# Optimization experiments

Measured on AMD Instinct MI355X. Metric: run time of the kernel, lower is better.

Reference implementation:

```python
import jax, jax.numpy as jnp
import numpy as np

NUM_HEADS = 16
NEG = -1e9

def setup_inputs() -> dict:
    key = jax.random.key(0)
    ks = jax.random.split(key, 5)
    B, S, D = 4, 2048, 1024
    scale = 1.0 / np.sqrt(D)
    return {
        "x": jax.random.normal(ks[0], (B, S, D), dtype=jnp.float32),
        "WQ": jax.random.normal(ks[1], (D, D), dtype=jnp.float32) * scale,
        "WK": jax.random.normal(ks[2], (D, D), dtype=jnp.float32) * scale,
        "WV": jax.random.normal(ks[3], (D, D), dtype=jnp.float32) * scale,
        "WO": jax.random.normal(ks[4], (D, D), dtype=jnp.float32) * scale,
    }

def _split_heads(t, h):
    # [..., s, h*d] -> [..., h, s, d]
    *lead, s, hd = t.shape
    return jnp.swapaxes(t.reshape(*lead, s, h, hd // h), -3, -2)

def reference(x, WQ, WK, WV, WO):
    h = NUM_HEADS
    S = x.shape[-2]
    # Linear stores weight [out, in]; y = x @ W^T
    Q = _split_heads(x @ WQ.T, h)  # [b,h,s,dk]
    K = _split_heads(x @ WK.T, h)
    V = _split_heads(x @ WV.T, h)
    dk = Q.shape[-1]
    scores = jnp.einsum('bhqd,bhkd->bhqk', Q, K) / jnp.sqrt(jnp.float32(dk))
    causal = jnp.tril(jnp.ones((S, S), dtype=bool))  # allowed positions
    scores = jnp.where(causal, scores, NEG)
    # explicit stable softmax (matches source)
    m = jnp.max(scores, axis=-1, keepdims=True)
    e = jnp.exp(scores - m)
    attn = e / jnp.sum(e, axis=-1, keepdims=True)
    out = jnp.einsum('bhqk,bhkd->bhqd', attn, V)  # [b,h,s,dv]
    out = jnp.swapaxes(out, -3, -2).reshape(*x.shape[:-1], -1)  # [b,s,h*dv]
    return out @ WO.T
```

## Files before the change

### kernel.cpp

```cpp
#include <hip/hip_runtime.h>
#include <stdint.h>
#include <math.h>

typedef __attribute__((ext_vector_type(8))) short bf16x8;
typedef __attribute__((ext_vector_type(4))) short v4s;
typedef __attribute__((ext_vector_type(4))) float f32x4;
typedef __attribute__((ext_vector_type(4))) unsigned short u16x4;
typedef __attribute__((ext_vector_type(2))) unsigned int u32x2;

#define MFMA16(a,b,c)   __builtin_amdgcn_mfma_f32_16x16x32_bf16((a),(b),(c),0,0,0)
#define MFMA16K(a,b,c)  __builtin_amdgcn_mfma_f32_16x16x16bf16_1k((a),(b),(c),0,0,0)

static __device__ __forceinline__ void gld_lds16(const void* g, void* l) {
  __builtin_amdgcn_global_load_lds(
      (const __attribute__((address_space(1))) unsigned int*)g,
      (__attribute__((address_space(3))) unsigned int*)l,
      16, 0, 0);
}

static __device__ __forceinline__ unsigned short f2bf(float f) {
  unsigned int u = __builtin_bit_cast(unsigned int, f);
  return (unsigned short)((u + 0x8000u) >> 16);
}

__global__ __launch_bounds__(256) void cvt_kernel(const float* __restrict__ in,
                                                  unsigned short* __restrict__ out,
                                                  int n4) {
  int i = blockIdx.x * blockDim.x + threadIdx.x;
  int stride = gridDim.x * blockDim.x;
  for (; i < n4; i += stride) {
    float4 v = ((const float4*)in)[i];
    u16x4 o;
    o.x = f2bf(v.x); o.y = f2bf(v.y); o.z = f2bf(v.z); o.w = f2bf(v.w);
    ((u16x4*)out)[i] = o;
  }
}

__global__ __launch_bounds__(256) void cvt4_kernel(const float* __restrict__ w0,
                                                   const float* __restrict__ w1,
                                                   const float* __restrict__ w2,
                                                   const float* __restrict__ w3,
                                                   unsigned short* __restrict__ out) {
  const float* in = (blockIdx.y == 0) ? w0 : (blockIdx.y == 1) ? w1
                  : (blockIdx.y == 2) ? w2 : w3;
  unsigned short* o = out + (size_t)blockIdx.y * 1048576;
  int i = blockIdx.x * blockDim.x + threadIdx.x;
  int stride = gridDim.x * blockDim.x;
  for (; i < 1048576/4; i += stride) {
    float4 v = ((const float4*)in)[i];
    u16x4 t;
    t.x = f2bf(v.x); t.y = f2bf(v.y); t.z = f2bf(v.z); t.w = f2bf(v.w);
    ((u16x4*)o)[i] = t;
  }
}

template<int MODE, typename CT>
__device__ __forceinline__ void gemm_bt_tile(const unsigned short* __restrict__ A,
                                             const unsigned short* __restrict__ Bt,
                                             CT* __restrict__ C,
                                             int m0, int n0)
{
  __shared__ __align__(16) unsigned short As[128*32];
  __shared__ __align__(16) unsigned short Bs[128*32];
  const int tid  = threadIdx.x;
  const int w    = tid >> 6, lane = tid & 63;
  const int quad = lane >> 4, c0 = lane & 15;
  const int wm   = w >> 1, wn = w & 1;

  const unsigned short* ga[2];
  const unsigned short* gb[2];
  int ldsoff[2];
  #pragma unroll
  for (int i = 0; i < 2; ++i) {
    int f = i*4096 + w*1024 + lane*16;
    int r = f >> 6;
    int q = (f >> 4) & 3;
    ga[i] = A  + (m0 + r)*1024 + q*8;
    gb[i] = Bt + (n0 + r)*1024 + q*8;
    ldsoff[i] = i*4096 + w*1024;
  }

  int aAddr[4], bAddr[4];
  #pragma unroll
  for (int t = 0; t < 4; ++t) {
    aAddr[t] = (wm*64 + t*16 + c0)*64 + quad*16;
    bAddr[t] = (wn*64 + t*16 + c0)*64 + quad*16;
  }

  f32x4 acc[4][4];
  #pragma unroll
  for (int i = 0; i < 4; ++i)
    #pragma unroll
    for (int j = 0; j < 4; ++j)
      acc[i][j] = (f32x4){0.f, 0.f, 0.f, 0.f};

  for (int kt = 0; kt < 32; ++kt) {
    __syncthreads();
    #pragma unroll
    for (int i = 0; i < 2; ++i) {
      gld_lds16(ga[i] + kt*32, (char*)As + ldsoff[i]);
      gld_lds16(gb[i] + kt*32, (char*)Bs + ldsoff[i]);
    }
    __syncthreads();

    bf16x8 af[4], bfr[4];
    #pragma unroll
    for (int t = 0; t < 4; ++t) af[t]  = *(const bf16x8*)((const char*)As + aAddr[t]);
    #pragma unroll
    for (int t = 0; t < 4; ++t) bfr[t] = *(const bf16x8*)((const char*)Bs + bAddr[t]);

    #pragma unroll
    for (int mt = 0; mt < 4; ++mt)
      #pragma unroll
      for (int nt = 0; nt < 4; ++nt)
        acc[mt][nt] = MFMA16(af[mt], bfr[nt], acc[mt][nt]);
  }

  const float scl = (MODE == 3) ? 0.1803368801f : 1.0f;
  #pragma unroll
  for (int mt = 0; mt < 4; ++mt) {
    #pragma unroll
    for (int nt = 0; nt < 4; ++nt) {
      if (MODE == 2) {
        u16x4 pk;
        #pragma unroll
        for (int r = 0; r < 4; ++r) pk[r] = f2bf(acc[mt][nt][r]);
        int s0 = m0 + wm*64 + mt*16 + quad*4;
        int gc = n0 + wn*64 + nt*16 + c0;
        int b = s0 >> 11, ss = s0 & 2047;
        int h = gc >> 6, d = gc & 63;
        *(u16x4*)((unsigned short*)C + (size_t)(((b << 4) + h)*64 + d)*2048 + ss) = pk;
      } else {
        #pragma unroll
        for (int r = 0; r < 4; ++r) {
          int gr = m0 + wm*64 + mt*16 + quad*4 + r;
          int gc = n0 + wn*64 + nt*16 + c0;
          if (MODE == 0 || MODE == 3) {
            int b = gr >> 11, s = gr & 2047;
            int h = gc >> 6, d = gc & 63;
            ((unsigned short*)C)[(((b << 4) + h)*2048 + s)*64 + d] = f2bf(acc[mt][nt][r] * scl);
          } else {
            ((float*)C)[gr*1024 + gc] = acc[mt][nt][r];
          }
        }
      }
    }
  }
}

__global__ __launch_bounds__(256) void qkv_kernel(
    const unsigned short* __restrict__ X,
    const unsigned short* __restrict__ WQ, const unsigned short* __restrict__ WK,
    const unsigned short* __restrict__ WV,
    unsigned short* __restrict__ Q, unsigned short* __restrict__ K,
    unsigned short* __restrict__ V)
{
  if (blockIdx.z == 2) {
    gemm_bt_tile<2>(X, WV, V, blockIdx.x*128, blockIdx.y*128);
  } else if (blockIdx.z == 0) {
    gemm_bt_tile<3>(X, WQ, Q, blockIdx.x*128, blockIdx.y*128);
  } else {
    gemm_bt_tile<0>(X, WK, K, blockIdx.x*128, blockIdx.y*128);
  }
}

__global__ __launch_bounds__(256) void proj_kernel(
    const unsigned short* __restrict__ A,
    const unsigned short* __restrict__ WO,
    float* __restrict__ C)
{
  gemm_bt_tile<1>(A, WO, C, blockIdx.x*128, blockIdx.y*128);
}

__global__ __launch_bounds__(256) void attn_kernel(
    const unsigned short* __restrict__ Q,
    const unsigned short* __restrict__ K,
    const unsigned short* __restrict__ Vt,
    unsigned short* __restrict__ O)
{
  __shared__ __align__(16) unsigned short VtL[2][64*128];

  const int tid  = threadIdx.x;
  const int w    = tid >> 6, lane = tid & 63;
  const int quad = lane >> 4, c0 = lane & 15;
  const int bx = blockIdx.x, bh = blockIdx.y;

  const unsigned short* Qh = Q  + (size_t)bh*2048*64;
  const unsigned short* Kh = K  + (size_t)bh*2048*64;
  const unsigned short* Vh = Vt + (size_t)bh*64*2048;

  const unsigned short* vga[4];
  int vldsoff[4];
  #pragma unroll
  for (int i = 0; i < 4; ++i) {
    int cid = i*256 + tid;
    int r = cid >> 4, q = cid & 15;
    int gq = q ^ (r & 15);
    vga[i] = Vh + (size_t)r*2048 + gq*8;
    vldsoff[i] = i*4096 + w*1024;
  }

  const int b = bh >> 4, h = bh & 15;
  bf16x8 kreg[8][2];

  #define ATTN_MK_BODY(mk, Vb, DIAG)                                              \
  {                                                                               \
    f32x4 s0 = (f32x4){0.f,0.f,0.f,0.f}, s1 = (f32x4){0.f,0.f,0.f,0.f};           \
    _Pragma("unroll")                                                             \
    for (int ks = 0; ks < 2; ++ks) {                                              \
      s0 = MFMA16(kreg[mk][ks], qf[0][ks], s0);                                   \
      s1 = MFMA16(kreg[mk][ks], qf[1][ks], s1);                                   \
    }                                                                             \
    if (DIAG) {                                                                   \
      _Pragma("unroll")                                                           \
      for (int r = 0; r < 4; ++r) {                                               \
        int kk = (mk)*16 + quad*4 + r;                                            \
        if (kk > w*32 + c0)      s0[r] = -1e30f;                                  \
        if (kk > w*32 + 16 + c0) s1[r] = -1e30f;                                  \
      }                                                                           \
    }                                                                             \
    float p00 = __builtin_amdgcn_exp2f(s0[0]), p01 = __builtin_amdgcn_exp2f(s0[1]); \
    float p02 = __builtin_amdgcn_exp2f(s0[2]), p03 = __builtin_amdgcn_exp2f(s0[3]); \
    float p10 = __builtin_amdgcn_exp2f(s1[0]), p11 = __builtin_amdgcn_exp2f(s1[1]); \
    float p12 = __builtin_amdgcn_exp2f(s1[2]), p13 = __builtin_amdgcn_exp2f(s1[3]); \
    l_r[0] += (p00 + p01) + (p02 + p03);                                          \
    l_r[1] += (p10 + p11) + (p12 + p13);                                          \
    u32x2 a0, a1;                                                                 \
    a0.x = __builtin_amdgcn_perm(__builtin_bit_cast(unsigned int, p01),           \
                                 __builtin_bit_cast(unsigned int, p00), 0x07060302u); \
    a0.y = __builtin_amdgcn_perm(__builtin_bit_cast(unsigned int, p03),           \
                                 __builtin_bit_cast(unsigned int, p02), 0x07060302u); \
    a1.x = __builtin_amdgcn_perm(__builtin_bit_cast(unsigned int, p11),           \
                                 __builtin_bit_cast(unsigned int, p10), 0x07060302u); \
    a1.y = __builtin_amdgcn_perm(__builtin_bit_cast(unsigned int, p13),           \
                                 __builtin_bit_cast(unsigned int, p12), 0x07060302u); \
    v4s pa0 = __builtin_bit_cast(v4s, a0);                                        \
    v4s pa1 = __builtin_bit_cast(v4s, a1);                                        \
    _Pragma("unroll")                                                             \
    for (int dt = 0; dt < 4; ++dt) {                                              \
      int vr = dt*16 + c0;                                                        \
      int p  = 2*(mk) + (quad >> 1);                                              \
      v4s vb = *(const v4s*)((const char*)(Vb) + vr*256 + ((p ^ c0) * 16) + (quad & 1)*8); \
      o_[0][dt] = MFMA16K(pa0, vb, o_[0][dt]);                                    \
      o_[1][dt] = MFMA16K(pa1, vb, o_[1][dt]);                                    \
    }                                                                             \
  }

  for (int pi = 0; pi < 2; ++pi) {
    const int qt = pi ? bx : 15 - bx;

    bf16x8 qf[2][2];
    #pragma unroll
    for (int mq = 0; mq < 2; ++mq)
      #pragma unroll
      for (int ks = 0; ks < 2; ++ks)
        qf[mq][ks] = *(const bf16x8*)(Qh + (qt*128 + w*32 + mq*16 + c0)*64 + ks*32 + quad*8);

    f32x4 o_[2][4];
    float l_r[2] = {0.f, 0.f};
    #pragma unroll
    for (int mq = 0; mq < 2; ++mq)
      #pragma unroll
      for (int dt = 0; dt < 4; ++dt) o_[mq][dt] = (f32x4){0.f, 0.f, 0.f, 0.f};

    __syncthreads();
    #pragma unroll
    for (int i = 0; i < 4; ++i)
      gld_lds16(vga[i], (char*)VtL[0] + vldsoff[i]);
    #pragma unroll
    for (int mk = 0; mk < 8; ++mk)
      #pragma unroll
      for (int ks = 0; ks < 2; ++ks)
        kreg[mk][ks] = *(const bf16x8*)(Kh + (mk*16 + c0)*64 + ks*32 + quad*8);

    for (int kt = 0; kt < qt; ++kt) {
      __syncthreads();
      #pragma unroll
      for (int i = 0; i < 4; ++i)
        gld_lds16(vga[i] + (kt+1)*128, (char*)VtL[(kt+1)&1] + vldsoff[i]);
      const unsigned short* Vb = VtL[kt & 1];
      #pragma unroll
      for (int mk = 0; mk < 8; ++mk)
        ATTN_MK_BODY(mk, Vb, false)
      #pragma unroll
      for (int mk = 0; mk < 8; ++mk)
        #pragma unroll
        for (int ks = 0; ks < 2; ++ks)
          kreg[mk][ks] = *(const bf16x8*)(Kh + ((kt+1)*128 + mk*16 + c0)*64 + ks*32 + quad*8);
    }

    {
      __syncthreads();
      const unsigned short* Vb = VtL[qt & 1];
      #pragma unroll
      for (int mk = 0; mk < 8; ++mk)
        if (mk < 2*w + 2)
          ATTN_MK_BODY(mk, Vb, true)
    }

    #pragma unroll
    for (int mq = 0; mq < 2; ++mq) {
      l_r[mq] += __shfl_xor(l_r[mq], 16);
      l_r[mq] += __shfl_xor(l_r[mq], 32);
    }
    #pragma unroll
    for (int mt = 0; mt < 2; ++mt) {
      #pragma unroll
      for (int r = 0; r < 4; ++r) {
        float l = __shfl(l_r[mt], quad*4 + r);
        float inv = 1.0f / l;
        int srow = qt*128 + w*32 + mt*16 + quad*4 + r;
        #pragma unroll
        for (int dt = 0; dt < 4; ++dt) {
          int col = h*64 + dt*16 + c0;
          O[((size_t)b*2048 + srow)*1024 + col] = f2bf(o_[mt][dt][r] * inv);
        }
      }
    }
  }
  #undef ATTN_MK_BODY
}

extern "C" void kernel_launch(void* const* d_in, const int* in_sizes, int n_in,
                              void* d_out, int out_size, void* d_ws, size_t ws_size,
                              hipStream_t stream) {
  const float* xf  = (const float*)d_in[0];
  const float* wqf = (const float*)d_in[1];
  const float* wkf = (const float*)d_in[2];
  const float* wvf = (const float*)d_in[3];
  const float* wof = (const float*)d_in[4];
  float* out = (float*)d_out;
  unsigned short* ws = (unsigned short*)d_ws;

  const bool fused = ws_size >= (size_t)58720256;

  if (fused) {
    unsigned short* xb  = ws;
    unsigned short* wb  = ws + 8388608;
    unsigned short* Kw  = ws + 12582912;
    unsigned short* Vw  = ws + 20971520;
    unsigned short* Ow  = xb;
    unsigned short* Qd  = (unsigned short*)out;

    cvt_kernel <<<2048, 256, 0, stream>>>(xf, xb, 8388608/4);
    cvt4_kernel<<<dim3(256, 4), 256, 0, stream>>>(wqf, wkf, wvf, wof, wb);

    qkv_kernel <<<dim3(64, 8, 3), 256, 0, stream>>>(xb, wb, wb + 1048576, wb + 2097152,
                                                    Qd, Kw, Vw);
    attn_kernel<<<dim3(8, 64),    256, 0, stream>>>(Qd, Kw, Vw, Ow);
    proj_kernel<<<dim3(64, 8),    256, 0, stream>>>(Ow, wb + 3145728, out);
  } else {
    unsigned short* xb  = ws;
    unsigned short* wb  = ws + 8388608;
    unsigned short* Kw  = ws + 12582912;
    unsigned short* Vw  = ws + 14680064;
    unsigned short* Ow  = ws + 16777216;

    cvt_kernel <<<2048, 256, 0, stream>>>(xf, xb, 8388608/4);
    cvt4_kernel<<<dim3(256, 4), 256, 0, stream>>>(wqf, wkf, wvf, wof, wb);

    for (int b = 0; b < 4; ++b) {
      const unsigned short* xbb = xb  + (size_t)b * 2048 * 1024;
      float*               outb = out + (size_t)b * 2048 * 1024;
      unsigned short*        Qd = (unsigned short*)outb;
      qkv_kernel <<<dim3(16, 8, 3), 256, 0, stream>>>(xbb, wb, wb + 1048576, wb + 2097152,
                                                      Qd, Kw, Vw);
      attn_kernel<<<dim3(8, 16),    256, 0, stream>>>(Qd, Kw, Vw, Ow);
      proj_kernel<<<dim3(16, 8),    256, 0, stream>>>(Ow, wb + 3145728, outb);
    }
  }
}
```

Baseline: 263.8 us.

## Halve attention query tile to 64 rows and merge conversion kernels

```diff
diff --git a/kernel.cpp b/kernel.cpp
--- a/kernel.cpp
+++ b/kernel.cpp
@@ -23,34 +23,28 @@
   return (unsigned short)((u + 0x8000u) >> 16);
 }
 
-__global__ __launch_bounds__(256) void cvt_kernel(const float* __restrict__ in,
-                                                  unsigned short* __restrict__ out,
-                                                  int n4) {
-  int i = blockIdx.x * blockDim.x + threadIdx.x;
-  int stride = gridDim.x * blockDim.x;
-  for (; i < n4; i += stride) {
-    float4 v = ((const float4*)in)[i];
+__global__ __launch_bounds__(256) void cvt_all_kernel(
+    const float* __restrict__ x,
+    const float* __restrict__ w0, const float* __restrict__ w1,
+    const float* __restrict__ w2, const float* __restrict__ w3,
+    unsigned short* __restrict__ xb, unsigned short* __restrict__ wb)
+{
+  int i = blockIdx.x * 256 + threadIdx.x;
+  const int stride = gridDim.x * 256;
+  for (; i < 3145728; i += stride) {
+    const float* src; unsigned short* dst; int off;
+    if (i < 2097152) { src = x; dst = xb; off = i; }
+    else {
+      int j = i - 2097152;
+      int seg = j >> 18;
+      off = j & 262143;
+      src = (seg == 0) ? w0 : (seg == 1) ? w1 : (seg == 2) ? w2 : w3;
+      dst = wb + (size_t)seg * 1048576;
+    }
+    float4 v = ((const float4*)src)[off];
     u16x4 o;
     o.x = f2bf(v.x); o.y = f2bf(v.y); o.z = f2bf(v.z); o.w = f2bf(v.w);
-    ((u16x4*)out)[i] = o;
-  }
-}
-
-__global__ __launch_bounds__(256) void cvt4_kernel(const float* __restrict__ w0,
-                                                   const float* __restrict__ w1,
-                                                   const float* __restrict__ w2,
-                                                   const float* __restrict__ w3,
-                                                   unsigned short* __restrict__ out) {
-  const float* in = (blockIdx.y == 0) ? w0 : (blockIdx.y == 1) ? w1
-                  : (blockIdx.y == 2) ? w2 : w3;
-  unsigned short* o = out + (size_t)blockIdx.y * 1048576;
-  int i = blockIdx.x * blockDim.x + threadIdx.x;
-  int stride = gridDim.x * blockDim.x;
-  for (; i < 1048576/4; i += stride) {
-    float4 v = ((const float4*)in)[i];
-    u16x4 t;
-    t.x = f2bf(v.x); t.y = f2bf(v.y); t.z = f2bf(v.z); t.w = f2bf(v.w);
-    ((u16x4*)o)[i] = t;
+    ((u16x4*)dst)[off] = o;
   }
 }
 
@@ -172,7 +166,7 @@
   gemm_bt_tile<1>(A, WO, C, blockIdx.x*128, blockIdx.y*128);
 }
 
-__global__ __launch_bounds__(256) void attn_kernel(
+__global__ __launch_bounds__(256, 4) void attn_kernel(
     const unsigned short* __restrict__ Q,
     const unsigned short* __restrict__ K,
     const unsigned short* __restrict__ Vt,
@@ -205,63 +199,49 @@
 
   #define ATTN_MK_BODY(mk, Vb, DIAG)                                              \
   {                                                                               \
-    f32x4 s0 = (f32x4){0.f,0.f,0.f,0.f}, s1 = (f32x4){0.f,0.f,0.f,0.f};           \
+    f32x4 s0 = (f32x4){0.f,0.f,0.f,0.f};                                          \
     _Pragma("unroll")                                                             \
-    for (int ks = 0; ks < 2; ++ks) {                                              \
-      s0 = MFMA16(kreg[mk][ks], qf[0][ks], s0);                                   \
-      s1 = MFMA16(kreg[mk][ks], qf[1][ks], s1);                                   \
-    }                                                                             \
+    for (int ks = 0; ks < 2; ++ks)                                                \
+      s0 = MFMA16(kreg[mk][ks], qf[ks], s0);                                      \
     if (DIAG) {                                                                   \
       _Pragma("unroll")                                                           \
       for (int r = 0; r < 4; ++r) {                                               \
         int kk = (mk)*16 + quad*4 + r;                                            \
-        if (kk > w*32 + c0)      s0[r] = -1e30f;                                  \
-        if (kk > w*32 + 16 + c0) s1[r] = -1e30f;                                  \
+        if (kk > qql) s0[r] = -1e30f;                                             \
       }                                                                           \
     }                                                                             \
-    float p00 = __builtin_amdgcn_exp2f(s0[0]), p01 = __builtin_amdgcn_exp2f(s0[1]); \
-    float p02 = __builtin_amdgcn_exp2f(s0[2]), p03 = __builtin_amdgcn_exp2f(s0[3]); \
-    float p10 = __builtin_amdgcn_exp2f(s1[0]), p11 = __builtin_amdgcn_exp2f(s1[1]); \
-    float p12 = __builtin_amdgcn_exp2f(s1[2]), p13 = __builtin_amdgcn_exp2f(s1[3]); \
-    l_r[0] += (p00 + p01) + (p02 + p03);                                          \
-    l_r[1] += (p10 + p11) + (p12 + p13);                                          \
-    u32x2 a0, a1;                                                                 \
-    a0.x = __builtin_amdgcn_perm(__builtin_bit_cast(unsigned int, p01),           \
-                                 __builtin_bit_cast(unsigned int, p00), 0x07060302u); \
-    a0.y = __builtin_amdgcn_perm(__builtin_bit_cast(unsigned int, p03),           \
-                                 __builtin_bit_cast(unsigned int, p02), 0x07060302u); \
-    a1.x = __builtin_amdgcn_perm(__builtin_bit_cast(unsigned int, p11),           \
-                                 __builtin_bit_cast(unsigned int, p10), 0x07060302u); \
-    a1.y = __builtin_amdgcn_perm(__builtin_bit_cast(unsigned int, p13),           \
-                                 __builtin_bit_cast(unsigned int, p12), 0x07060302u); \
+    float p0 = __builtin_amdgcn_exp2f(s0[0]), p1 = __builtin_amdgcn_exp2f(s0[1]); \
+    float p2 = __builtin_amdgcn_exp2f(s0[2]), p3 = __builtin_amdgcn_exp2f(s0[3]); \
+    l_r += (p0 + p1) + (p2 + p3);                                                 \
+    u32x2 a0;                                                                     \
+    a0.x = __builtin_amdgcn_perm(__builtin_bit_cast(unsigned int, p1),            \
+                                 __builtin_bit_cast(unsigned int, p0), 0x07060302u); \
+    a0.y = __builtin_amdgcn_perm(__builtin_bit_cast(unsigned int, p3),            \
+                                 __builtin_bit_cast(unsigned int, p2), 0x07060302u); \
     v4s pa0 = __builtin_bit_cast(v4s, a0);                                        \
-    v4s pa1 = __builtin_bit_cast(v4s, a1);                                        \
     _Pragma("unroll")                                                             \
     for (int dt = 0; dt < 4; ++dt) {                                              \
       int vr = dt*16 + c0;                                                        \
       int p  = 2*(mk) + (quad >> 1);                                              \
       v4s vb = *(const v4s*)((const char*)(Vb) + vr*256 + ((p ^ c0) * 16) + (quad & 1)*8); \
-      o_[0][dt] = MFMA16K(pa0, vb, o_[0][dt]);                                    \
-      o_[1][dt] = MFMA16K(pa1, vb, o_[1][dt]);                                    \
+      o_[dt] = MFMA16K(pa0, vb, o_[dt]);                                          \
     }                                                                             \
   }
 
   for (int pi = 0; pi < 2; ++pi) {
-    const int qt = pi ? bx : 15 - bx;
-
-    bf16x8 qf[2][2];
-    #pragma unroll
-    for (int mq = 0; mq < 2; ++mq)
-      #pragma unroll
-      for (int ks = 0; ks < 2; ++ks)
-        qf[mq][ks] = *(const bf16x8*)(Qh + (qt*128 + w*32 + mq*16 + c0)*64 + ks*32 + quad*8);
-
-    f32x4 o_[2][4];
-    float l_r[2] = {0.f, 0.f};
-    #pragma unroll
-    for (int mq = 0; mq < 2; ++mq)
-      #pragma unroll
-      for (int dt = 0; dt < 4; ++dt) o_[mq][dt] = (f32x4){0.f, 0.f, 0.f, 0.f};
+    const int qc = pi ? bx : 31 - bx;
+    const int D  = qc >> 1;
+    const int qql = (qc & 1)*64 + w*16 + c0;
+
+    bf16x8 qf[2];
+    #pragma unroll
+    for (int ks = 0; ks < 2; ++ks)
+      qf[ks] = *(const bf16x8*)(Qh + (qc*64 + w*16 + c0)*64 + ks*32 + quad*8);
+
+    f32x4 o_[4];
+    float l_r = 0.f;
+    #pragma unroll
+    for (int dt = 0; dt < 4; ++dt) o_[dt] = (f32x4){0.f, 0.f, 0.f, 0.f};
 
     __syncthreads();
     #pragma unroll
@@ -273,7 +253,7 @@
       for (int ks = 0; ks < 2; ++ks)
         kreg[mk][ks] = *(const bf16x8*)(Kh + (mk*16 + c0)*64 + ks*32 + quad*8);
 
-    for (int kt = 0; kt < qt; ++kt) {
+    for (int kt = 0; kt < D; ++kt) {
       __syncthreads();
       #pragma unroll
       for (int i = 0; i < 4; ++i)
@@ -291,30 +271,26 @@
 
     {
       __syncthreads();
-      const unsigned short* Vb = VtL[qt & 1];
+      const unsigned short* Vb = VtL[D & 1];
+      const int mkEnd = ((qc & 1) << 2) + w + 1;
       #pragma unroll
       for (int mk = 0; mk < 8; ++mk)
-        if (mk < 2*w + 2)
+        if (mk < mkEnd)
           ATTN_MK_BODY(mk, Vb, true)
     }
 
-    #pragma unroll
-    for (int mq = 0; mq < 2; ++mq) {
-      l_r[mq] += __shfl_xor(l_r[mq], 16);
-      l_r[mq] += __shfl_xor(l_r[mq], 32);
-    }
-    #pragma unroll
-    for (int mt = 0; mt < 2; ++mt) {
-      #pragma unroll
-      for (int r = 0; r < 4; ++r) {
-        float l = __shfl(l_r[mt], quad*4 + r);
-        float inv = 1.0f / l;
-        int srow = qt*128 + w*32 + mt*16 + quad*4 + r;
-        #pragma unroll
-        for (int dt = 0; dt < 4; ++dt) {
-          int col = h*64 + dt*16 + c0;
-          O[((size_t)b*2048 + srow)*1024 + col] = f2bf(o_[mt][dt][r] * inv);
-        }
+    l_r += __shfl_xor(l_r, 16);
+    l_r += __shfl_xor(l_r, 32);
+
+    #pragma unroll
+    for (int r = 0; r < 4; ++r) {
+      float l = __shfl(l_r, quad*4 + r);
+      float inv = 1.0f / l;
+      int srow = qc*64 + w*16 + quad*4 + r;
+      #pragma unroll
+      for (int dt = 0; dt < 4; ++dt) {
+        int col = h*64 + dt*16 + c0;
+        O[((size_t)b*2048 + srow)*1024 + col] = f2bf(o_[dt][r] * inv);
       }
     }
   }
@@ -342,12 +318,11 @@
     unsigned short* Ow  = xb;
     unsigned short* Qd  = (unsigned short*)out;
 
-    cvt_kernel <<<2048, 256, 0, stream>>>(xf, xb, 8388608/4);
-    cvt4_kernel<<<dim3(256, 4), 256, 0, stream>>>(wqf, wkf, wvf, wof, wb);
+    cvt_all_kernel<<<3072, 256, 0, stream>>>(xf, wqf, wkf, wvf, wof, xb, wb);
 
     qkv_kernel <<<dim3(64, 8, 3), 256, 0, stream>>>(xb, wb, wb + 1048576, wb + 2097152,
                                                     Qd, Kw, Vw);
-    attn_kernel<<<dim3(8, 64),    256, 0, stream>>>(Qd, Kw, Vw, Ow);
+    attn_kernel<<<dim3(16, 64),   256, 0, stream>>>(Qd, Kw, Vw, Ow);
     proj_kernel<<<dim3(64, 8),    256, 0, stream>>>(Ow, wb + 3145728, out);
   } else {
     unsigned short* xb  = ws;
@@ -356,8 +331,7 @@
     unsigned short* Vw  = ws + 14680064;
     unsigned short* Ow  = ws + 16777216;
 
-    cvt_kernel <<<2048, 256, 0, stream>>>(xf, xb, 8388608/4);
-    cvt4_kernel<<<dim3(256, 4), 256, 0, stream>>>(wqf, wkf, wvf, wof, wb);
+    cvt_all_kernel<<<3072, 256, 0, stream>>>(xf, wqf, wkf, wvf, wof, xb, wb);
 
     for (int b = 0; b < 4; ++b) {
       const unsigned short* xbb = xb  + (size_t)b * 2048 * 1024;
@@ -365,7 +339,7 @@
       unsigned short*        Qd = (unsigned short*)outb;
       qkv_kernel <<<dim3(16, 8, 3), 256, 0, stream>>>(xbb, wb, wb + 1048576, wb + 2097152,
                                                       Qd, Kw, Vw);
-      attn_kernel<<<dim3(8, 16),    256, 0, stream>>>(Qd, Kw, Vw, Ow);
+      attn_kernel<<<dim3(16, 16),   256, 0, stream>>>(Qd, Kw, Vw, Ow);
       proj_kernel<<<dim3(16, 8),    256, 0, stream>>>(Ow, wb + 3145728, outb);
     }
   }
```

Result: slower. 341.6 us (+29.5%).
